# Kernel tuning notes

Measured on AMD Instinct MI355X. Metric: run time of the kernel, lower is better.

The kernel has to match this reference:

```python
import jax, jax.numpy as jnp
from jax import lax
import numpy as np

B, C, H, W = 32, 256, 16, 16          # batch, planes, feature-map HxW
NBUF, REPS, LAB = 100000, 256, 10     # buffer size, reps dim, label dim
D = REPS + LAB                        # retrieval_data feature dim
DH = 64                               # cross_dim_head (heads=1 -> inner=64)
INNER = DH
EPS = 1e-5


def _ln(x, g, b):
    m = x.mean(-1, keepdims=True)
    v = ((x - m) ** 2).mean(-1, keepdims=True)
    return (x - m) * lax.rsqrt(v + EPS) * g + b


def _conv(x, w):
    return lax.conv_general_dilated(x, w, (1, 1), 'SAME',
                                    dimension_numbers=('NCHW', 'OIHW', 'NCHW'))


def _forward(x, conv1_w, conv2_w, bn1_g, bn1_b, bn2_g, bn2_b, retrieval_data,
             ln_attn_g, ln_attn_b, ln_ctx_g, ln_ctx_b, wq, wk, wv, wqe, wo, bo,
             ln_ff_g, ln_ff_b, w1, b1, w2, b2, topk):
    # eval-mode BatchNorm with running mean=0, var=1
    bn = lambda y, g, b: y * g[None, :, None, None] + b[None, :, None, None]
    out = jax.nn.relu(bn(_conv(x, conv1_w), bn1_g, bn1_b))
    out = bn(_conv(out, conv2_w), bn2_g, bn2_b)
    out = jax.nn.relu(out + x)                        # identity shortcut
    t = out.reshape(B, C, H * W).transpose(0, 2, 1)   # [B, n, C] tokens

    # ---- retrieval cross-attention (PreNorm on x and on context) ----
    xn = _ln(t, ln_attn_g, ln_attn_b)
    ctx = _ln(retrieval_data, ln_ctx_g, ln_ctx_b)     # [NBUF, D]
    q = xn @ wq                                        # [B, n, INNER]
    emb = q @ wqe                                      # [B, n, REPS]
    e0 = emb[:, 0, :]                                  # original loop only uses position 0
    buf_reps = ctx[:, :REPS]                           # [NBUF, REPS]
    # squared L2 has the same ordering as the L2 norm used by torch.topk(largest=False)
    dist2 = jnp.sum((buf_reps[None] - e0[:, None]) ** 2, axis=-1)  # [B, NBUF]
    idx = lax.top_k(-dist2, topk)[1]                   # [B, topk] nearest indices
    retrieved = jnp.take(ctx, idx, axis=0)             # [B, topk, D]; identical for all n positions
    reps_r, labels_r = retrieved[..., :REPS], retrieved[..., REPS:]
    k = reps_r @ wk                                    # reps_for_k: K from reps  [B, topk, INNER]
    v = labels_r @ wv                                  # V from labels            [B, topk, INNER]
    sim = jnp.einsum('bnd,bjd->bnj', q, k) * DH ** -0.5
    attn = jax.nn.softmax(sim, axis=-1)
    o = jnp.einsum('bnj,bjd->bnd', attn, v)
    t = o @ wo + bo + t

    # ---- feed-forward (PreNorm, GEGLU, mult=1) ----
    h = _ln(t, ln_ff_g, ln_ff_b) @ w1 + b1             # [B, n, 2C]
    a, g = jnp.split(h, 2, axis=-1)
    t = (a * jax.nn.gelu(g, approximate=False)) @ w2 + b2 + t

    return t.transpose(0, 2, 1).reshape(B, C, H, W)


def setup_inputs() -> dict:
    key = jax.random.key(0)
    ks = jax.random.split(key, 12)
    s = 0.02
    return {
        'x': jax.random.normal(ks[0], (B, C, H, W), jnp.float32),
        'conv1_w': jax.random.normal(ks[1], (C, C, 3, 3), jnp.float32) * s,
        'conv2_w': jax.random.normal(ks[2], (C, C, 3, 3), jnp.float32) * s,
        'bn1_g': jnp.ones((C,), jnp.float32), 'bn1_b': jnp.zeros((C,), jnp.float32),
        'bn2_g': jnp.ones((C,), jnp.float32), 'bn2_b': jnp.zeros((C,), jnp.float32),
        'retrieval_data': jax.random.normal(ks[3], (NBUF, D), jnp.float32),
        'ln_attn_g': jnp.ones((C,), jnp.float32), 'ln_attn_b': jnp.zeros((C,), jnp.float32),
        'ln_ctx_g': jnp.ones((D,), jnp.float32), 'ln_ctx_b': jnp.zeros((D,), jnp.float32),
        'wq': jax.random.normal(ks[4], (C, INNER), jnp.float32) * s,
        'wk': jax.random.normal(ks[5], (REPS, INNER), jnp.float32) * s,
        'wv': jax.random.normal(ks[6], (LAB, INNER), jnp.float32) * s,
        'wqe': jax.random.normal(ks[7], (INNER, REPS), jnp.float32) * s,
        'wo': jax.random.normal(ks[8], (INNER, C), jnp.float32) * s,
        'bo': jnp.zeros((C,), jnp.float32),
        'ln_ff_g': jnp.ones((C,), jnp.float32), 'ln_ff_b': jnp.zeros((C,), jnp.float32),
        'w1': jax.random.normal(ks[9], (C, 2 * C), jnp.float32) * s,
        'b1': jnp.zeros((2 * C,), jnp.float32),
        'w2': jax.random.normal(ks[10], (C, C), jnp.float32) * s,
        'b2': jnp.zeros((C,), jnp.float32),
        'topk': 32,
    }


def reference(x, conv1_w, conv2_w, bn1_g, bn1_b, bn2_g, bn2_b, retrieval_data,
              ln_attn_g, ln_attn_b, ln_ctx_g, ln_ctx_b, wq, wk, wv, wqe, wo, bo,
              ln_ff_g, ln_ff_b, w1, b1, w2, b2, topk):
    return _forward(x, conv1_w, conv2_w, bn1_g, bn1_b, bn2_g, bn2_b, retrieval_data,
                    ln_attn_g, ln_attn_b, ln_ctx_g, ln_ctx_b, wq, wk, wv, wqe, wo, bo,
                    ln_ff_g, ln_ff_b, w1, b1, w2, b2, topk)
```

## Files before the change

kernel.cpp:

```cpp
#include <hip/hip_runtime.h>
#include <hip/hip_bf16.h>
#include <math.h>

#define DEV __device__ __forceinline__

typedef __attribute__((ext_vector_type(8))) short bf16x8;
typedef __attribute__((ext_vector_type(4))) float f32x4;
typedef __attribute__((ext_vector_type(4))) unsigned int u32x4;
typedef __attribute__((ext_vector_type(2))) unsigned int u32x2;

DEV float b2f(unsigned int u) { return __uint_as_float(u << 16); }
DEV unsigned short f2b(float f) {
    unsigned int x = __float_as_uint(f);
    unsigned int r = x + 0x7fffu + ((x >> 16) & 1u);
    return (unsigned short)(r >> 16);
}
DEV unsigned int pack2(float a, float b) {
    return (unsigned int)f2b(a) | ((unsigned int)f2b(b) << 16);
}
DEV float gelu_exact(float g) {
    return 0.5f * g * (1.f + erff(g * 0.70710678118654752f));
}

constexpr size_t WP1  = 0;
// ... 170 lines not shown
        float g = bng[co], bb = bnb[co];
#pragma unroll
        for (int r = 0; r < 4; ++r) {
            int m = m0 + mt * 16 + lq * 4 + r;
            int h = m >> 4, w = m & 15;
            float v = sum[r] * g + bb;
            if (EPI == 0) {
                v = fmaxf(v, 0.f);
                outP[((size_t)img * 324 + (h + 1) * 18 + (w + 1)) * 256 + co] = f2b(v);
            } else {
                v += b2f(resid[((size_t)img * 324 + (h + 1) * 18 + (w + 1)) * 256 + co]);
                v = fmaxf(v, 0.f);
                outT[((size_t)img * 256 + m) * 256 + co] = v;
            }
        }
    }
}

__global__ __launch_bounds__(256) void lnq_k(
    const float* __restrict__ t, const float* __restrict__ g, const float* __restrict__ bta,
    const unsigned short* __restrict__ bpq, const float* __restrict__ wqe,
    unsigned short* __restrict__ qb, unsigned short* __restrict__ e0p)
{
    __shared__ __align__(16) unsigned int frag[64 * 132];
    __shared__ float qrow[64];
    int bx = blockIdx.x, tid = threadIdx.x;
    int wv = tid >> 6, lane = tid & 63;
    int c = lane * 4;
    f32x4 gv = *(const f32x4*)(g + c);
    f32x4 bv = *(const f32x4*)(bta + c);
#pragma unroll
    for (int p = 0; p < 16; ++p) {
        int rl = wv * 16 + p;
        f32x4 x = *(const f32x4*)(t + (size_t)(bx * 64 + rl) * 256 + c);
        float s  = x[0] + x[1] + x[2] + x[3];
        float ss = x[0]*x[0] + x[1]*x[1] + x[2]*x[2] + x[3]*x[3];
#pragma unroll
        for (int off = 32; off >= 1; off >>= 1) { s += __shfl_xor(s, off); ss += __shfl_xor(ss, off); }
        float mean = s * (1.f / 256.f);
        float var  = ss * (1.f / 256.f) - mean * mean;
        float rstd = rsqrtf(fmaxf(var, 0.f) + 1e-5f);
        float y0 = (x[0]-mean)*rstd*gv[0] + bv[0];
        float y1 = (x[1]-mean)*rstd*gv[1] + bv[1];
        float y2 = (x[2]-mean)*rstd*gv[2] + bv[2];
        float y3 = (x[3]-mean)*rstd*gv[3] + bv[3];
        frag[rl * 132 + 2 * lane]     = pack2(y0, y1);
        frag[rl * 132 + 2 * lane + 1] = pack2(y2, y3);
    }
    __syncthreads();
    int lq = lane >> 4, lr = lane & 15;
    f32x4 acc[4];
#pragma unroll
    for (int nt = 0; nt < 4; ++nt) acc[nt] = 0.f;
    const short* sA = (const short*)frag;
#pragma unroll
    for (int kc = 0; kc < 8; ++kc) {
        bf16x8 a = *(const bf16x8*)(sA + (wv * 16 + lr) * 264 + kc * 32 + lq * 8);
#pragma unroll
        for (int nt = 0; nt < 4; ++nt) {
            bf16x8 bfr = *(const bf16x8*)(bpq + (size_t)(kc * 4 + nt) * 512 + lane * 8);
            acc[nt] = __builtin_amdgcn_mfma_f32_16x16x32_bf16(a, bfr, acc[nt], 0, 0, 0);
        }
    }
#pragma unroll
    for (int nt = 0; nt < 4; ++nt)
#pragma unroll
        for (int r = 0; r < 4; ++r)
            qb[(size_t)(bx * 64 + wv * 16 + lq * 4 + r) * 64 + nt * 16 + lr] = f2b(acc[nt][r]);
    if ((bx & 3) == 0 && wv == 0 && lq == 0) {
#pragma unroll
        for (int nt = 0; nt < 4; ++nt) qrow[nt * 16 + lr] = acc[nt][0];
    }
    __syncthreads();
    if ((bx & 3) == 0) {
        int b = bx >> 2;
        int r = tid;
        float a2 = 0.f;
#pragma unroll 8
        for (int d = 0; d < 64; ++d) a2 += qrow[d] * wqe[d * 256 + r];
        int nt = b >> 4, kc = r >> 5;
        int ln_ = (b & 15) + (((r >> 3) & 3) << 4);
        int j = r & 7;
        e0p[(((nt * 8 + kc) * 64) + ln_) * 8 + j] = f2b(a2);
    }
}

__global__ __launch_bounds__(256, 4) void lndist_k(
    const float* __restrict__ ctx, const float* __restrict__ lgam, const float* __restrict__ lbet,
    const unsigned short* __restrict__ e0p, float* __restrict__ dist)
{
    __shared__ __align__(16) unsigned int frag[32 * 132];
    __shared__ __align__(16) float rn2s[32];
    int r0 = blockIdx.x * 32;
    int tid = threadIdx.x;
    int wv = tid >> 6, lane = tid & 63;

    float2 d0[8], d1[8], d2[8];
    const float* base = ctx + (size_t)(r0 + wv * 8) * 266;
#pragma unroll
    for (int p = 0; p < 8; ++p) {
        const float* rowp = base + p * 266;
        d0[p] = *(const float2*)(rowp + 2 * lane);
        d1[p] = *(const float2*)(rowp + 128 + 2 * lane);
        if (lane < 5) d2[p] = *(const float2*)(rowp + 256 + 2 * lane);
        else { d2[p].x = 0.f; d2[p].y = 0.f; }
    }
    float2 g0 = *(const float2*)(lgam + 2 * lane);
    float2 g1 = *(const float2*)(lgam + 128 + 2 * lane);
    float2 b0 = *(const float2*)(lbet + 2 * lane);
    float2 b1 = *(const float2*)(lbet + 128 + 2 * lane);

#pragma unroll
    for (int p = 0; p < 8; ++p) {
        int rl = wv * 8 + p;
        float s  = d0[p].x + d0[p].y + d1[p].x + d1[p].y + d2[p].x + d2[p].y;
        float ss = d0[p].x*d0[p].x + d0[p].y*d0[p].y + d1[p].x*d1[p].x + d1[p].y*d1[p].y
                 + d2[p].x*d2[p].x + d2[p].y*d2[p].y;
#pragma unroll
        for (int off = 32; off >= 1; off >>= 1) { s += __shfl_xor(s, off); ss += __shfl_xor(ss, off); }
        float mean = s * (1.f / 266.f);
        float var  = ss * (1.f / 266.f) - mean * mean;
        float rstd = rsqrtf(fmaxf(var, 0.f) + 1e-5f);
        float c0 = (d0[p].x - mean) * rstd * g0.x + b0.x;
        float c1 = (d0[p].y - mean) * rstd * g0.y + b0.y;
        float c2 = (d1[p].x - mean) * rstd * g1.x + b1.x;
        float c3 = (d1[p].y - mean) * rstd * g1.y + b1.y;
        frag[rl * 132 + lane]      = pack2(c0, c1);
        frag[rl * 132 + 64 + lane] = pack2(c2, c3);
        float nsq = c0*c0 + c1*c1 + c2*c2 + c3*c3;
#pragma unroll
        for (int off = 32; off >= 1; off >>= 1) nsq += __shfl_xor(nsq, off);
        if (lane == 0) rn2s[rl] = nsq;
    }
    __syncthreads();

    int lq = lane >> 4, lr = lane & 15;
    int rt = wv & 1, ch = wv >> 1;
    f32x4 acc = 0.f;
    const short* sA = (const short*)frag;
#pragma unroll
    for (int kc = 0; kc < 8; ++kc) {
        bf16x8 a = *(const bf16x8*)(sA + (rt * 16 + lr) * 264 + kc * 32 + lq * 8);
        bf16x8 b = *(const bf16x8*)(e0p + ((ch * 8 + kc) * 64 + lane) * 8);
        acc = __builtin_amdgcn_mfma_f32_16x16x32_bf16(a, b, acc, 0, 0, 0);
    }
    int mbase = r0 + rt * 16 + lq * 4;
    f32x4 rv = *(f32x4*)(rn2s + rt * 16 + lq * 4);
    f32x4 o;
#pragma unroll
    for (int r = 0; r < 4; ++r) o[r] = rv[r] - 2.f * acc[r];
    *(f32x4*)(dist + (size_t)(ch * 16 + lr) * 100000 + mbase) = o;
}

__global__ __launch_bounds__(256) void topk1(const float* __restrict__ dist,
                                             float* __restrict__ candv,
                                             int* __restrict__ candi)
{
    __shared__ float sv[6250];
    __shared__ float wvv[4]; __shared__ int wvi[4];
    int c = blockIdx.x, b = blockIdx.y;
    int tid = threadIdx.x;
    const float* src = dist + (size_t)b * 100000 + c * 6250;
    for (int i = tid; i < 6250; i += 256) sv[i] = src[i];
    __syncthreads();
    for (int it = 0; it < 32; ++it) {
        float lm = 3e38f; int li = 0;
        for (int i = tid; i < 6250; i += 256) {
            float v = sv[i];
            if (v < lm) { lm = v; li = i; }
        }
#pragma unroll
        for (int off = 32; off >= 1; off >>= 1) {
            float ov = __shfl_xor(lm, off);
            int oi = __shfl_xor(li, off);
            if (ov < lm) { lm = ov; li = oi; }
        }
        if ((tid & 63) == 0) { wvv[tid >> 6] = lm; wvi[tid >> 6] = li; }
        __syncthreads();
        if (tid == 0) {
            float m = wvv[0]; int mi = wvi[0];
#pragma unroll
            for (int w = 1; w < 4; ++w) if (wvv[w] < m) { m = wvv[w]; mi = wvi[w]; }
            candv[((size_t)b * 16 + c) * 32 + it] = m;
            candi[((size_t)b * 16 + c) * 32 + it] = c * 6250 + mi;
            sv[mi] = 3e38f;
        }
        __syncthreads();
    }
}

__global__ __launch_bounds__(256) void topk2(const float* __restrict__ candv,
                                             const int* __restrict__ candi,
                                             int* __restrict__ idxo)
{
    __shared__ float sv[512]; __shared__ int si[512];
    __shared__ float wvv[4]; __shared__ int wvi[4];
    int b = blockIdx.x, tid = threadIdx.x;
    for (int i = tid; i < 512; i += 256) { sv[i] = candv[(size_t)b * 512 + i]; si[i] = candi[(size_t)b * 512 + i]; }
    __syncthreads();
    for (int it = 0; it < 32; ++it) {
        float lm = 3e38f; int li = 0;
#pragma unroll
        for (int rep = 0; rep < 2; ++rep) {
            int i = tid + rep * 256;
            float v = sv[i];
            if (v < lm) { lm = v; li = i; }
        }
#pragma unroll
        for (int off = 32; off >= 1; off >>= 1) {
            float ov = __shfl_xor(lm, off);
            int oi = __shfl_xor(li, off);
            if (ov < lm) { lm = ov; li = oi; }
        }
        if ((tid & 63) == 0) { wvv[tid >> 6] = lm; wvi[tid >> 6] = li; }
        __syncthreads();
        if (tid == 0) {
            float m = wvv[0]; int mi = wvi[0];
#pragma unroll
            for (int w = 1; w < 4; ++w) if (wvv[w] < m) { m = wvv[w]; mi = wvi[w]; }
            idxo[b * 32 + it] = si[mi];
            sv[mi] = 3e38f;
        }
        __syncthreads();
    }
}

__global__ __launch_bounds__(64) void gather_kv(const float* __restrict__ ctx,
                                                const float* __restrict__ g,
                                                const float* __restrict__ b,
                                                const int* __restrict__ idxb,
                                                const float* __restrict__ wk,
                                                const float* __restrict__ wvm,
                                                float* __restrict__ kb,
                                                float* __restrict__ vb)
{
    __shared__ float cnv[266];
    int bj = blockIdx.x;
    int lane = threadIdx.x;
    int row = idxb[bj];
    const float* p = ctx + (size_t)row * 266;
    float2 a0 = *(const float2*)(p + 2 * lane);
    float2 a1 = *(const float2*)(p + 128 + 2 * lane);
    float x4 = 0.f, x5 = 0.f;
    if (lane < 5) { float2 a2 = *(const float2*)(p + 256 + 2 * lane); x4 = a2.x; x5 = a2.y; }
    float s  = a0.x + a0.y + a1.x + a1.y + x4 + x5;
    float ss = a0.x*a0.x + a0.y*a0.y + a1.x*a1.x + a1.y*a1.y + x4*x4 + x5*x5;
#pragma unroll
    for (int off = 32; off >= 1; off >>= 1) { s += __shfl_xor(s, off); ss += __shfl_xor(ss, off); }
    float mean = s * (1.f / 266.f);
    float var  = ss * (1.f / 266.f) - mean * mean;
    float rstd = rsqrtf(fmaxf(var, 0.f) + 1e-5f);
    float2 g0 = *(const float2*)(g + 2 * lane);
    float2 g1 = *(const float2*)(g + 128 + 2 * lane);
    float2 b0 = *(const float2*)(b + 2 * lane);
    float2 b1 = *(const float2*)(b + 128 + 2 * lane);
    cnv[2*lane]       = (a0.x - mean) * rstd * g0.x + b0.x;
    cnv[2*lane + 1]   = (a0.y - mean) * rstd * g0.y + b0.y;
    cnv[128 + 2*lane] = (a1.x - mean) * rstd * g1.x + b1.x;
    cnv[129 + 2*lane] = (a1.y - mean) * rstd * g1.y + b1.y;
    if (lane < 5) {
        float2 g2 = *(const float2*)(g + 256 + 2 * lane);
        float2 b2 = *(const float2*)(b + 256 + 2 * lane);
        cnv[256 + 2*lane] = (x4 - mean) * rstd * g2.x + b2.x;
        cnv[257 + 2*lane] = (x5 - mean) * rstd * g2.y + b2.y;
    }
    __syncthreads();
    float acc = 0.f;
#pragma unroll 8
    for (int r = 0; r < 256; ++r) acc += cnv[r] * wk[r * 64 + lane];
    kb[(size_t)bj * 64 + lane] = acc;
    float acc2 = 0.f;
#pragma unroll
    for (int r = 0; r < 10; ++r) acc2 += cnv[256 + r] * wvm[r * 64 + lane];
    vb[(size_t)bj * 64 + lane] = acc2;
}

__global__ __launch_bounds__(256) void attn_k(const unsigned short* __restrict__ q,
                                              const float* __restrict__ kb,
                                              const float* __restrict__ vb,
                                              unsigned short* __restrict__ ob)
{
    __shared__ float kl[32 * 66];
    __shared__ float vl[32 * 66];
    __shared__ float ql[8 * 64];
    __shared__ float pl[8 * 32];
    int b = blockIdx.x >> 5, pxg = blockIdx.x & 31;
    int px_base = pxg * 8;
    int tid = threadIdx.x;

    for (int i = tid; i < 2048; i += 256) {
        int row = i >> 6, d = i & 63;
        kl[row * 66 + d] = kb[(size_t)b * 2048 + i];
        vl[row * 66 + d] = vb[(size_t)b * 2048 + i];
    }
    for (int i = tid; i < 512; i += 256) {
        ql[i] = b2f(q[((size_t)b * 256 + px_base) * 64 + i]);
    }
    __syncthreads();

    int wv = tid >> 6, lane = tid & 63;
    int lp = wv * 2 + (lane >> 5);
    int j = lane & 31;

    const float* qp = ql + lp * 64;
    const float* kp = kl + j * 66;
    float s = 0.f;
#pragma unroll
    for (int d = 0; d < 64; ++d) s += qp[d] * kp[d];
    s *= 0.125f;

    float mx = s;
#pragma unroll
    for (int off = 16; off >= 1; off >>= 1) mx = fmaxf(mx, __shfl_xor(mx, off));
    float p = expf(s - mx);
    float sum = p;
#pragma unroll
    for (int off = 16; off >= 1; off >>= 1) sum += __shfl_xor(sum, off);
    p /= sum;
    pl[lp * 32 + j] = p;

    int d0 = 2 * j;
    float o0 = 0.f, o1 = 0.f;
#pragma unroll
    for (int jj = 0; jj < 32; ++jj) {
        float pj = pl[lp * 32 + jj];
        float2 vv = *(const float2*)(vl + jj * 66 + d0);
        o0 += pj * vv.x;
        o1 += pj * vv.y;
    }
    ((unsigned int*)ob)[(((size_t)b * 256 + px_base + lp) * 64 + d0) >> 1] = pack2(o0, o1);
}

__global__ __launch_bounds__(256) void wo_ln_k(
    const unsigned short* __restrict__ A, const unsigned short* __restrict__ Bp,
    const float* __restrict__ bo, const float* __restrict__ tres,
    float* __restrict__ t2, unsigned short* __restrict__ xn2,
    const float* __restrict__ lng, const float* __restrict__ lnb)
{
    __shared__ __align__(16) float tile[32 * 268];
    int m0 = blockIdx.x * 32;
    int tid = threadIdx.x, wv = tid >> 6, lane = tid & 63, lq = lane >> 4, lr = lane & 15;
    int n0 = wv * 64;
    f32x4 acc[2][4];
#pragma unroll
    for (int i = 0; i < 2; ++i)
#pragma unroll
        for (int j = 0; j < 4; ++j) acc[i][j] = 0.f;
    const unsigned short* a0p = A + (size_t)(m0 + lr) * 64 + lq * 8;
#pragma unroll
    for (int kc = 0; kc < 2; ++kc) {
        bf16x8 a0 = *(const bf16x8*)(a0p + kc * 32);
        bf16x8 a1 = *(const bf16x8*)(a0p + 16 * 64 + kc * 32);
#pragma unroll
        for (int nt = 0; nt < 4; ++nt) {
            bf16x8 bfr = *(const bf16x8*)(Bp + (size_t)(kc * 16 + (n0 >> 4) + nt) * 512 + lane * 8);
            acc[0][nt] = __builtin_amdgcn_mfma_f32_16x16x32_bf16(a0, bfr, acc[0][nt], 0, 0, 0);
            acc[1][nt] = __builtin_amdgcn_mfma_f32_16x16x32_bf16(a1, bfr, acc[1][nt], 0, 0, 0);
        }
    }
#pragma unroll
    for (int mt = 0; mt < 2; ++mt)
#pragma unroll
        for (int nt = 0; nt < 4; ++nt)
#pragma unroll
            for (int r = 0; r < 4; ++r)
                tile[(mt * 16 + lq * 4 + r) * 268 + n0 + nt * 16 + lr] = acc[mt][nt][r];
    __syncthreads();
    int row = tid >> 3, c0 = (tid & 7) * 32;
    const float* trp = tres + (size_t)(m0 + row) * 256 + c0;
    float v[32];
#pragma unroll
    for (int i = 0; i < 8; ++i) {
        f32x4 t4 = *(f32x4*)(tile + row * 268 + c0 + i * 4);
        f32x4 rr = *(const f32x4*)(trp + i * 4);
        f32x4 bb = *(const f32x4*)(bo + c0 + i * 4);
#pragma unroll
        for (int k = 0; k < 4; ++k) v[i*4+k] = t4[k] + rr[k] + bb[k];
    }
    float* t2p = t2 + (size_t)(m0 + row) * 256 + c0;
#pragma unroll
    for (int i = 0; i < 8; ++i) {
        f32x4 o; o[0] = v[i*4]; o[1] = v[i*4+1]; o[2] = v[i*4+2]; o[3] = v[i*4+3];
        *(f32x4*)(t2p + i * 4) = o;
    }
    float s = 0.f, ss = 0.f;
#pragma unroll
    for (int i = 0; i < 32; ++i) { s += v[i]; ss += v[i] * v[i]; }
#pragma unroll
    for (int off = 1; off <= 4; off <<= 1) { s += __shfl_xor(s, off); ss += __shfl_xor(ss, off); }
    float mean = s * (1.f / 256.f);
    float var  = ss * (1.f / 256.f) - mean * mean;
    float rstd = rsqrtf(fmaxf(var, 0.f) + 1e-5f);
    unsigned int pk[16];
#pragma unroll
    for (int i = 0; i < 16; ++i) {
        float y0 = (v[2*i]   - mean) * rstd * lng[c0+2*i]   + lnb[c0+2*i];
        float y1 = (v[2*i+1] - mean) * rstd * lng[c0+2*i+1] + lnb[c0+2*i+1];
        pk[i] = pack2(y0, y1);
    }
    u32x4* dp = (u32x4*)(xn2 + (size_t)(m0 + row) * 256 + c0);
#pragma unroll
    for (int i = 0; i < 4; ++i) {
        u32x4 o; o.x = pk[i*4]; o.y = pk[i*4+1]; o.z = pk[i*4+2]; o.w = pk[i*4+3];
        dp[i] = o;
    }
}

__global__ __launch_bounds__(256) void ff1_k(
    const unsigned short* __restrict__ A, const unsigned short* __restrict__ Bp,
    const float* __restrict__ b1, unsigned short* __restrict__ u)
{
    __shared__ __align__(16) float tile[64 * 68];
    int m0 = blockIdx.x * 64, by = blockIdx.y;
    int tid = threadIdx.x, wv = tid >> 6, lane = tid & 63, lq = lane >> 4, lr = lane & 15;
    int mh = wv & 1, sel = wv >> 1;
    int m0w = m0 + mh * 32;
    int nbase = sel * 256 + by * 32;
    f32x4 acc[2][2];
#pragma unroll
    for (int i = 0; i < 2; ++i)
#pragma unroll
        for (int j = 0; j < 2; ++j) acc[i][j] = 0.f;
    const unsigned short* a0p = A + (size_t)(m0w + lr) * 256 + lq * 8;
#pragma unroll
    for (int kc = 0; kc < 8; ++kc) {
        bf16x8 a0 = *(const bf16x8*)(a0p + kc * 32);
        bf16x8 a1 = *(const bf16x8*)(a0p + 16 * 256 + kc * 32);
#pragma unroll
        for (int nt = 0; nt < 2; ++nt) {
            bf16x8 bfr = *(const bf16x8*)(Bp + (size_t)(kc * 32 + (nbase >> 4) + nt) * 512 + lane * 8);
            acc[0][nt] = __builtin_amdgcn_mfma_f32_16x16x32_bf16(a0, bfr, acc[0][nt], 0, 0, 0);
            acc[1][nt] = __builtin_amdgcn_mfma_f32_16x16x32_bf16(a1, bfr, acc[1][nt], 0, 0, 0);
        }
    }
#pragma unroll
    for (int nt = 0; nt < 2; ++nt) {
        float bias = b1[nbase + nt * 16 + lr];
#pragma unroll
        for (int mt = 0; mt < 2; ++mt)
#pragma unroll
            for (int r = 0; r < 4; ++r)
                tile[(mh * 32 + mt * 16 + lq * 4 + r) * 68 + sel * 32 + nt * 16 + lr] = acc[mt][nt][r] + bias;
    }
    __syncthreads();
    int row = tid >> 2, c0 = (tid & 3) * 8;
    unsigned int pk[4];
#pragma unroll
    for (int i = 0; i < 4; ++i) {
        float a0 = tile[row * 68 + c0 + 2*i];
        float a1 = tile[row * 68 + c0 + 2*i + 1];
        float g0 = tile[row * 68 + 32 + c0 + 2*i];
        float g1 = tile[row * 68 + 32 + c0 + 2*i + 1];
        pk[i] = pack2(a0 * gelu_exact(g0), a1 * gelu_exact(g1));
    }
    u32x4 o; o.x = pk[0]; o.y = pk[1]; o.z = pk[2]; o.w = pk[3];
    *(u32x4*)(u + (size_t)(m0 + row) * 256 + by * 32 + c0) = o;
}

__global__ __launch_bounds__(256) void ff2_k(
    const unsigned short* __restrict__ A, const unsigned short* __restrict__ Bp,
    const float* __restrict__ b2, const float* __restrict__ t2,
    float* __restrict__ out)
{
    __shared__ __align__(16) float tile[64 * 68];
    int m0 = blockIdx.x * 64, n0 = blockIdx.y * 64;
    int tid = threadIdx.x, wv = tid >> 6, lane = tid & 63, lq = lane >> 4, lr = lane & 15;
    int mq = wv & 1, nq = wv >> 1;
    int m0w = m0 + mq * 32, n0w = n0 + nq * 32;
    f32x4 acc[2][2];
#pragma unroll
    for (int i = 0; i < 2; ++i)
#pragma unroll
        for (int j = 0; j < 2; ++j) acc[i][j] = 0.f;
    const unsigned short* a0p = A + (size_t)(m0w + lr) * 256 + lq * 8;
#pragma unroll
    for (int kc = 0; kc < 8; ++kc) {
        bf16x8 a0 = *(const bf16x8*)(a0p + kc * 32);
        bf16x8 a1 = *(const bf16x8*)(a0p + 16 * 256 + kc * 32);
#pragma unroll
        for (int nt = 0; nt < 2; ++nt) {
            bf16x8 bfr = *(const bf16x8*)(Bp + (size_t)(kc * 16 + (n0w >> 4) + nt) * 512 + lane * 8);
            acc[0][nt] = __builtin_amdgcn_mfma_f32_16x16x32_bf16(a0, bfr, acc[0][nt], 0, 0, 0);
            acc[1][nt] = __builtin_amdgcn_mfma_f32_16x16x32_bf16(a1, bfr, acc[1][nt], 0, 0, 0);
        }
    }
#pragma unroll
    for (int nt = 0; nt < 2; ++nt) {
        int col = n0w + nt * 16 + lr;
        float bv = b2[col];
#pragma unroll
        for (int mt = 0; mt < 2; ++mt)
#pragma unroll
            for (int r = 0; r < 4; ++r) {
                int m = m0w + mt * 16 + lq * 4 + r;
                tile[(mq * 32 + mt * 16 + lq * 4 + r) * 68 + nq * 32 + nt * 16 + lr] =
                    acc[mt][nt][r] + bv + t2[(size_t)m * 256 + col];
            }
    }
    __syncthreads();
    int b = m0 >> 8, px0 = m0 & 255;
    int cl = tid >> 2, pc = (tid & 3) * 16;
    float* dp = out + ((size_t)b * 256 + n0 + cl) * 256 + px0 + pc;
#pragma unroll
    for (int i = 0; i < 4; ++i) {
        f32x4 o;
        o[0] = tile[(pc + i * 4 + 0) * 68 + cl];
        o[1] = tile[(pc + i * 4 + 1) * 68 + cl];
        o[2] = tile[(pc + i * 4 + 2) * 68 + cl];
        o[3] = tile[(pc + i * 4 + 3) * 68 + cl];
        *(f32x4*)(dp + i * 4) = o;
    }
}

extern "C" void kernel_launch(void* const* d_in, const int* in_sizes, int n_in,
                              void* d_out, int out_size, void* d_ws, size_t ws_size,
                              hipStream_t stream)
{
    (void)in_sizes; (void)n_in; (void)out_size; (void)ws_size;
    const float* x    = (const float*)d_in[0];
    const float* c1w  = (const float*)d_in[1];
    const float* c2w  = (const float*)d_in[2];
    const float* bn1g = (const float*)d_in[3];
    const float* bn1b = (const float*)d_in[4];
    const float* bn2g = (const float*)d_in[5];
    const float* bn2b = (const float*)d_in[6];
    const float* rdat = (const float*)d_in[7];
    const float* lag  = (const float*)d_in[8];
    const float* labp = (const float*)d_in[9];
    const float* lcg  = (const float*)d_in[10];
    const float* lcb  = (const float*)d_in[11];
    const float* wq   = (const float*)d_in[12];
    const float* wk   = (const float*)d_in[13];
    const float* wv   = (const float*)d_in[14];
    const float* wqe  = (const float*)d_in[15];
    const float* wo   = (const float*)d_in[16];
    const float* bo   = (const float*)d_in[17];
    const float* lfg  = (const float*)d_in[18];
    const float* lfb  = (const float*)d_in[19];
    const float* w1   = (const float*)d_in[20];
    const float* b1   = (const float*)d_in[21];
    const float* w2   = (const float*)d_in[22];
    const float* b2   = (const float*)d_in[23];

    char* ws = (char*)d_ws;
    unsigned short* wp1  = (unsigned short*)(ws + WP1);
    unsigned short* wp2  = (unsigned short*)(ws + WP2);
    unsigned short* bpq  = (unsigned short*)(ws + BPQ);
    unsigned short* bpo  = (unsigned short*)(ws + BPO);
    unsigned short* bp1  = (unsigned short*)(ws + BP1);
    unsigned short* bp2  = (unsigned short*)(ws + BP2);
    unsigned short* xtp  = (unsigned short*)(ws + XTP);
    unsigned short* o1p  = (unsigned short*)(ws + O1P);
    float*          tb   = (float*)(ws + TBUF);
    unsigned short* qb   = (unsigned short*)(ws + QB);
    unsigned short* e0p  = (unsigned short*)(ws + E0P);
    float*          dist = (float*)(ws + DIST);
    float*          cdv  = (float*)(ws + CANDV);
    int*            cdi  = (int*)(ws + CANDI);
    int*            idxb = (int*)(ws + IDXB);
    float*          kb   = (float*)(ws + KBF);
    float*          vbuf = (float*)(ws + VBF);
    unsigned short* ob   = (unsigned short*)(ws + OBF);
    float*          t2   = (float*)(ws + T2B);
    unsigned short* xn2  = (unsigned short*)(ws + XN2);
    unsigned short* ub   = (unsigned short*)(ws + UBF);
    float*          outp = (float*)d_out;

    setup_k<<<944, 256, 0, stream>>>(x, c1w, c2w, wq, wo, w1, w2,
                                     wp1, wp2, bpq, bpo, bp1, bp2, xtp, o1p);
    conv_mfma<0><<<512, 256, 0, stream>>>(xtp, wp1, bn1g, bn1b, nullptr, o1p, nullptr);
    conv_mfma<1><<<512, 256, 0, stream>>>(o1p, wp2, bn2g, bn2b, xtp, nullptr, tb);
    lnq_k<<<128, 256, 0, stream>>>(tb, lag, labp, bpq, wqe, qb, e0p);
    lndist_k<<<3125, 256, 0, stream>>>(rdat, lcg, lcb, e0p, dist);
    topk1<<<dim3(16, 32), 256, 0, stream>>>(dist, cdv, cdi);
    topk2<<<32, 256, 0, stream>>>(cdv, cdi, idxb);
    gather_kv<<<1024, 64, 0, stream>>>(rdat, lcg, lcb, idxb, wk, wv, kb, vbuf);
    attn_k<<<1024, 256, 0, stream>>>(qb, kb, vbuf, ob);
    wo_ln_k<<<256, 256, 0, stream>>>(ob, bpo, bo, tb, t2, xn2, lfg, lfb);
    ff1_k<<<dim3(128, 8), 256, 0, stream>>>(xn2, bp1, b1, ub);
    ff2_k<<<dim3(128, 4), 256, 0, stream>>>(ub, bp2, b2, t2, outp);
}
```

Measured before the change: 397.7 us.

## Use per-wave top-k selection and fuse select/gather and the FFN tail

The first top-k stage now lets each of the four waves in a block pick its own 32 smallest values from a 1600-element slice, using only wave barriers. This removes the per-iteration block barriers and the serial thread-0 merge, at the cost of four times as many candidates. The second top-k stage, the context LayerNorm gather and the K/V projections are merged into one kernel per batch, and the K projection reuses each weight load across 8 rows. The Wo projection with residual and LayerNorm, FF1 with GELU gating, and FF2 with residual and transposed store are fused into one kernel that keeps intermediates in LDS. This cuts launches and global round trips, but the fused tail runs only 256 blocks and uses more LDS per block.

```diff
diff --git a/kernel.cpp b/kernel.cpp
--- a/kernel.cpp
+++ b/kernel.cpp
@@ -346,20 +346,26 @@
     *(f32x4*)(dist + (size_t)(ch * 16 + lr) * 100000 + mbase) = o;
 }
 
-__global__ __launch_bounds__(256) void topk1(const float* __restrict__ dist,
-                                             float* __restrict__ candv,
-                                             int* __restrict__ candi)
-{
-    __shared__ float sv[6250];
-    __shared__ float wvv[4]; __shared__ int wvi[4];
+__global__ __launch_bounds__(256) void topk1w(const float* __restrict__ dist,
+                                              float* __restrict__ candv,
+                                              int* __restrict__ candi)
+{
+    __shared__ float sv[6400];
     int c = blockIdx.x, b = blockIdx.y;
     int tid = threadIdx.x;
+    int wv = tid >> 6, lane = tid & 63;
     const float* src = dist + (size_t)b * 100000 + c * 6250;
     for (int i = tid; i < 6250; i += 256) sv[i] = src[i];
-    __syncthreads();
+    for (int i = 6250 + tid; i < 6400; i += 256) sv[i] = 3e38f;
+    __syncthreads();
+    int base = wv * 1600;
+    float* cvp = candv + (((size_t)b * 16 + c) * 4 + wv) * 32;
+    int*   cip = candi + (((size_t)b * 16 + c) * 4 + wv) * 32;
     for (int it = 0; it < 32; ++it) {
-        float lm = 3e38f; int li = 0;
-        for (int i = tid; i < 6250; i += 256) {
+        float lm = 3e38f; int li = base;
+#pragma unroll
+        for (int t = 0; t < 25; ++t) {
+            int i = base + lane + t * 64;
             float v = sv[i];
             if (v < lm) { lm = v; li = i; }
         }
@@ -369,104 +375,135 @@
             int oi = __shfl_xor(li, off);
             if (ov < lm) { lm = ov; li = oi; }
         }
-        if ((tid & 63) == 0) { wvv[tid >> 6] = lm; wvi[tid >> 6] = li; }
-        __syncthreads();
-        if (tid == 0) {
-            float m = wvv[0]; int mi = wvi[0];
-#pragma unroll
-            for (int w = 1; w < 4; ++w) if (wvv[w] < m) { m = wvv[w]; mi = wvi[w]; }
-            candv[((size_t)b * 16 + c) * 32 + it] = m;
-            candi[((size_t)b * 16 + c) * 32 + it] = c * 6250 + mi;
-            sv[mi] = 3e38f;
-        }
-        __syncthreads();
-    }
-}
-
-__global__ __launch_bounds__(256) void topk2(const float* __restrict__ candv,
-                                             const int* __restrict__ candi,
-                                             int* __restrict__ idxo)
-{
-    __shared__ float sv[512]; __shared__ int si[512];
-    __shared__ float wvv[4]; __shared__ int wvi[4];
+        if (lane == 0) {
+            cvp[it] = lm;
+            cip[it] = c * 6250 + li;
+            sv[li] = 3e38f;
+        }
+        __builtin_amdgcn_wave_barrier();
+    }
+}
+
+__global__ __launch_bounds__(256) void selkv_k(const float* __restrict__ candv,
+                                               const int* __restrict__ candi,
+                                               const float* __restrict__ ctx,
+                                               const float* __restrict__ g,
+                                               const float* __restrict__ bta,
+                                               const float* __restrict__ wk,
+                                               const float* __restrict__ wvm,
+                                               float* __restrict__ kb,
+                                               float* __restrict__ vb)
+{
+    __shared__ float sv[2048]; __shared__ int si[2048];
+    __shared__ float fv[128];  __shared__ int fi[128];
+    __shared__ int rows[32];
+    __shared__ float cnv[32][268];
     int b = blockIdx.x, tid = threadIdx.x;
-    for (int i = tid; i < 512; i += 256) { sv[i] = candv[(size_t)b * 512 + i]; si[i] = candi[(size_t)b * 512 + i]; }
-    __syncthreads();
-    for (int it = 0; it < 32; ++it) {
-        float lm = 3e38f; int li = 0;
-#pragma unroll
-        for (int rep = 0; rep < 2; ++rep) {
-            int i = tid + rep * 256;
-            float v = sv[i];
-            if (v < lm) { lm = v; li = i; }
-        }
-#pragma unroll
-        for (int off = 32; off >= 1; off >>= 1) {
-            float ov = __shfl_xor(lm, off);
-            int oi = __shfl_xor(li, off);
-            if (ov < lm) { lm = ov; li = oi; }
-        }
-        if ((tid & 63) == 0) { wvv[tid >> 6] = lm; wvi[tid >> 6] = li; }
-        __syncthreads();
-        if (tid == 0) {
-            float m = wvv[0]; int mi = wvi[0];
-#pragma unroll
-            for (int w = 1; w < 4; ++w) if (wvv[w] < m) { m = wvv[w]; mi = wvi[w]; }
-            idxo[b * 32 + it] = si[mi];
-            sv[mi] = 3e38f;
-        }
-        __syncthreads();
-    }
-}
-
-__global__ __launch_bounds__(64) void gather_kv(const float* __restrict__ ctx,
-                                                const float* __restrict__ g,
-                                                const float* __restrict__ b,
-                                                const int* __restrict__ idxb,
-                                                const float* __restrict__ wk,
-                                                const float* __restrict__ wvm,
-                                                float* __restrict__ kb,
-                                                float* __restrict__ vb)
-{
-    __shared__ float cnv[266];
-    int bj = blockIdx.x;
-    int lane = threadIdx.x;
-    int row = idxb[bj];
-    const float* p = ctx + (size_t)row * 266;
-    float2 a0 = *(const float2*)(p + 2 * lane);
-    float2 a1 = *(const float2*)(p + 128 + 2 * lane);
-    float x4 = 0.f, x5 = 0.f;
-    if (lane < 5) { float2 a2 = *(const float2*)(p + 256 + 2 * lane); x4 = a2.x; x5 = a2.y; }
-    float s  = a0.x + a0.y + a1.x + a1.y + x4 + x5;
-    float ss = a0.x*a0.x + a0.y*a0.y + a1.x*a1.x + a1.y*a1.y + x4*x4 + x5*x5;
-#pragma unroll
-    for (int off = 32; off >= 1; off >>= 1) { s += __shfl_xor(s, off); ss += __shfl_xor(ss, off); }
-    float mean = s * (1.f / 266.f);
-    float var  = ss * (1.f / 266.f) - mean * mean;
-    float rstd = rsqrtf(fmaxf(var, 0.f) + 1e-5f);
-    float2 g0 = *(const float2*)(g + 2 * lane);
-    float2 g1 = *(const float2*)(g + 128 + 2 * lane);
-    float2 b0 = *(const float2*)(b + 2 * lane);
-    float2 b1 = *(const float2*)(b + 128 + 2 * lane);
-    cnv[2*lane]       = (a0.x - mean) * rstd * g0.x + b0.x;
-    cnv[2*lane + 1]   = (a0.y - mean) * rstd * g0.y + b0.y;
-    cnv[128 + 2*lane] = (a1.x - mean) * rstd * g1.x + b1.x;
-    cnv[129 + 2*lane] = (a1.y - mean) * rstd * g1.y + b1.y;
-    if (lane < 5) {
-        float2 g2 = *(const float2*)(g + 256 + 2 * lane);
-        float2 b2 = *(const float2*)(b + 256 + 2 * lane);
-        cnv[256 + 2*lane] = (x4 - mean) * rstd * g2.x + b2.x;
-        cnv[257 + 2*lane] = (x5 - mean) * rstd * g2.y + b2.y;
-    }
-    __syncthreads();
-    float acc = 0.f;
-#pragma unroll 8
-    for (int r = 0; r < 256; ++r) acc += cnv[r] * wk[r * 64 + lane];
-    kb[(size_t)bj * 64 + lane] = acc;
-    float acc2 = 0.f;
-#pragma unroll
-    for (int r = 0; r < 10; ++r) acc2 += cnv[256 + r] * wvm[r * 64 + lane];
-    vb[(size_t)bj * 64 + lane] = acc2;
+    int wv = tid >> 6, lane = tid & 63;
+    for (int i = tid; i < 2048; i += 256) {
+        sv[i] = candv[(size_t)b * 2048 + i];
+        si[i] = candi[(size_t)b * 2048 + i];
+    }
+    __syncthreads();
+    {
+        int base = wv * 512;
+        for (int it = 0; it < 32; ++it) {
+            float lm = 3e38f; int li = base;
+#pragma unroll
+            for (int t = 0; t < 8; ++t) {
+                int i = base + lane + t * 64;
+                float v = sv[i];
+                if (v < lm) { lm = v; li = i; }
+            }
+#pragma unroll
+            for (int off = 32; off >= 1; off >>= 1) {
+                float ov = __shfl_xor(lm, off);
+                int oi = __shfl_xor(li, off);
+                if (ov < lm) { lm = ov; li = oi; }
+            }
+            if (lane == 0) { fv[wv * 32 + it] = lm; fi[wv * 32 + it] = si[li]; sv[li] = 3e38f; }
+            __builtin_amdgcn_wave_barrier();
+        }
+    }
+    __syncthreads();
+    if (wv == 0) {
+        for (int it = 0; it < 32; ++it) {
+            float lm = 3e38f; int li = 0;
+#pragma unroll
+            for (int t = 0; t < 2; ++t) {
+                int i = lane + t * 64;
+                float v = fv[i];
+                if (v < lm) { lm = v; li = i; }
+            }
+#pragma unroll
+            for (int off = 32; off >= 1; off >>= 1) {
+                float ov = __shfl_xor(lm, off);
+                int oi = __shfl_xor(li, off);
+                if (ov < lm) { lm = ov; li = oi; }
+            }
+            if (lane == 0) { rows[it] = fi[li]; fv[li] = 3e38f; }
+            __builtin_amdgcn_wave_barrier();
+        }
+    }
+    __syncthreads();
+    for (int p = 0; p < 8; ++p) {
+        int j = wv * 8 + p;
+        int rrow = rows[j];
+        const float* pp = ctx + (size_t)rrow * 266;
+        float2 a0 = *(const float2*)(pp + 2 * lane);
+        float2 a1 = *(const float2*)(pp + 128 + 2 * lane);
+        float x4 = 0.f, x5 = 0.f;
+        if (lane < 5) { float2 a2 = *(const float2*)(pp + 256 + 2 * lane); x4 = a2.x; x5 = a2.y; }
+        float s  = a0.x + a0.y + a1.x + a1.y + x4 + x5;
+        float ss = a0.x*a0.x + a0.y*a0.y + a1.x*a1.x + a1.y*a1.y + x4*x4 + x5*x5;
+#pragma unroll
+        for (int off = 32; off >= 1; off >>= 1) { s += __shfl_xor(s, off); ss += __shfl_xor(ss, off); }
+        float mean = s * (1.f / 266.f);
+        float var  = ss * (1.f / 266.f) - mean * mean;
+        float rstd = rsqrtf(fmaxf(var, 0.f) + 1e-5f);
+        float2 g0 = *(const float2*)(g + 2 * lane);
+        float2 g1 = *(const float2*)(g + 128 + 2 * lane);
+        float2 b0 = *(const float2*)(bta + 2 * lane);
+        float2 b1 = *(const float2*)(bta + 128 + 2 * lane);
+        cnv[j][2*lane]       = (a0.x - mean) * rstd * g0.x + b0.x;
+        cnv[j][2*lane + 1]   = (a0.y - mean) * rstd * g0.y + b0.y;
+        cnv[j][128 + 2*lane] = (a1.x - mean) * rstd * g1.x + b1.x;
+        cnv[j][129 + 2*lane] = (a1.y - mean) * rstd * g1.y + b1.y;
+        if (lane < 5) {
+            float2 g2 = *(const float2*)(g + 256 + 2 * lane);
+            float2 b2 = *(const float2*)(bta + 256 + 2 * lane);
+            cnv[j][256 + 2*lane] = (x4 - mean) * rstd * g2.x + b2.x;
+            cnv[j][257 + 2*lane] = (x5 - mean) * rstd * g2.y + b2.y;
+        }
+    }
+    __syncthreads();
+    {
+        float acc[8];
+#pragma unroll
+        for (int p = 0; p < 8; ++p) acc[p] = 0.f;
+        int j0 = wv * 8;
+        for (int r = 0; r < 256; r += 4) {
+            float w0 = wk[(r + 0) * 64 + lane];
+            float w1_ = wk[(r + 1) * 64 + lane];
+            float w2_ = wk[(r + 2) * 64 + lane];
+            float w3 = wk[(r + 3) * 64 + lane];
+#pragma unroll
+            for (int p = 0; p < 8; ++p) {
+                f32x4 cv = *(const f32x4*)&cnv[j0 + p][r];
+                acc[p] += cv[0] * w0 + cv[1] * w1_ + cv[2] * w2_ + cv[3] * w3;
+            }
+        }
+#pragma unroll
+        for (int p = 0; p < 8; ++p)
+            kb[((size_t)b * 32 + j0 + p) * 64 + lane] = acc[p];
+#pragma unroll
+        for (int p = 0; p < 8; ++p) {
+            float a2 = 0.f;
+#pragma unroll
+            for (int r = 0; r < 10; ++r) a2 += cnv[j0 + p][256 + r] * wvm[r * 64 + lane];
+            vb[((size_t)b * 32 + j0 + p) * 64 + lane] = a2;
+        }
+    }
 }
 
 __global__ __launch_bounds__(256) void attn_k(const unsigned short* __restrict__ q,
@@ -525,184 +562,171 @@
     ((unsigned int*)ob)[(((size_t)b * 256 + px_base + lp) * 64 + d0) >> 1] = pack2(o0, o1);
 }
 
-__global__ __launch_bounds__(256) void wo_ln_k(
-    const unsigned short* __restrict__ A, const unsigned short* __restrict__ Bp,
+__global__ __launch_bounds__(256) void tail_k(
+    const unsigned short* __restrict__ A,
+    const unsigned short* __restrict__ Bpo,
     const float* __restrict__ bo, const float* __restrict__ tres,
-    float* __restrict__ t2, unsigned short* __restrict__ xn2,
-    const float* __restrict__ lng, const float* __restrict__ lnb)
+    const float* __restrict__ lng, const float* __restrict__ lnb,
+    const unsigned short* __restrict__ Bp1, const float* __restrict__ b1,
+    const unsigned short* __restrict__ Bp2, const float* __restrict__ b2,
+    float* __restrict__ out)
 {
     __shared__ __align__(16) float tile[32 * 268];
+    __shared__ __align__(16) unsigned short xt[32 * 264];
     int m0 = blockIdx.x * 32;
     int tid = threadIdx.x, wv = tid >> 6, lane = tid & 63, lq = lane >> 4, lr = lane & 15;
     int n0 = wv * 64;
-    f32x4 acc[2][4];
+    const short* xts = (const short*)xt;
+
+    {
+        f32x4 acc[2][4];
+#pragma unroll
+        for (int i = 0; i < 2; ++i)
+#pragma unroll
+            for (int j = 0; j < 4; ++j) acc[i][j] = 0.f;
+        const unsigned short* a0p = A + (size_t)(m0 + lr) * 64 + lq * 8;
+#pragma unroll
+        for (int kc = 0; kc < 2; ++kc) {
+            bf16x8 a0 = *(const bf16x8*)(a0p + kc * 32);
+            bf16x8 a1 = *(const bf16x8*)(a0p + 16 * 64 + kc * 32);
+#pragma unroll
+            for (int nt = 0; nt < 4; ++nt) {
+                bf16x8 bfr = *(const bf16x8*)(Bpo + (size_t)(kc * 16 + (n0 >> 4) + nt) * 512 + lane * 8);
+                acc[0][nt] = __builtin_amdgcn_mfma_f32_16x16x32_bf16(a0, bfr, acc[0][nt], 0, 0, 0);
+                acc[1][nt] = __builtin_amdgcn_mfma_f32_16x16x32_bf16(a1, bfr, acc[1][nt], 0, 0, 0);
+            }
+        }
+#pragma unroll
+        for (int mt = 0; mt < 2; ++mt)
+#pragma unroll
+            for (int nt = 0; nt < 4; ++nt)
+#pragma unroll
+                for (int r = 0; r < 4; ++r)
+                    tile[(mt * 16 + lq * 4 + r) * 268 + n0 + nt * 16 + lr] = acc[mt][nt][r];
+    }
+    __syncthreads();
+
+    {
+        int row = tid >> 3, c0 = (tid & 7) * 32;
+        const float* trp = tres + (size_t)(m0 + row) * 256 + c0;
+        float v[32];
+#pragma unroll
+        for (int i = 0; i < 8; ++i) {
+            f32x4 t4 = *(f32x4*)(tile + row * 268 + c0 + i * 4);
+            f32x4 rr = *(const f32x4*)(trp + i * 4);
+            f32x4 bb = *(const f32x4*)(bo + c0 + i * 4);
+#pragma unroll
+            for (int k = 0; k < 4; ++k) v[i*4+k] = t4[k] + rr[k] + bb[k];
+        }
+#pragma unroll
+        for (int i = 0; i < 8; ++i) {
+            f32x4 o; o[0] = v[i*4]; o[1] = v[i*4+1]; o[2] = v[i*4+2]; o[3] = v[i*4+3];
+            *(f32x4*)(tile + row * 268 + c0 + i * 4) = o;
+        }
+        float s = 0.f, ss = 0.f;
+#pragma unroll
+        for (int i = 0; i < 32; ++i) { s += v[i]; ss += v[i] * v[i]; }
+#pragma unroll
+        for (int off = 1; off <= 4; off <<= 1) { s += __shfl_xor(s, off); ss += __shfl_xor(ss, off); }
+        float mean = s * (1.f / 256.f);
+        float var  = ss * (1.f / 256.f) - mean * mean;
+        float rstd = rsqrtf(fmaxf(var, 0.f) + 1e-5f);
+        unsigned int pk[16];
+#pragma unroll
+        for (int i = 0; i < 16; ++i) {
+            float y0 = (v[2*i]   - mean) * rstd * lng[c0+2*i]   + lnb[c0+2*i];
+            float y1 = (v[2*i+1] - mean) * rstd * lng[c0+2*i+1] + lnb[c0+2*i+1];
+            pk[i] = pack2(y0, y1);
+        }
+        u32x4* dp = (u32x4*)(xt + row * 264 + c0);
+#pragma unroll
+        for (int i = 0; i < 4; ++i) {
+            u32x4 o; o.x = pk[i*4]; o.y = pk[i*4+1]; o.z = pk[i*4+2]; o.w = pk[i*4+3];
+            dp[i] = o;
+        }
+    }
+    __syncthreads();
+
+    f32x4 fa[2][4], fg[2][4];
 #pragma unroll
     for (int i = 0; i < 2; ++i)
 #pragma unroll
-        for (int j = 0; j < 4; ++j) acc[i][j] = 0.f;
-    const unsigned short* a0p = A + (size_t)(m0 + lr) * 64 + lq * 8;
-#pragma unroll
-    for (int kc = 0; kc < 2; ++kc) {
-        bf16x8 a0 = *(const bf16x8*)(a0p + kc * 32);
-        bf16x8 a1 = *(const bf16x8*)(a0p + 16 * 64 + kc * 32);
+        for (int j = 0; j < 4; ++j) { fa[i][j] = 0.f; fg[i][j] = 0.f; }
+#pragma unroll
+    for (int kc = 0; kc < 8; ++kc) {
+        bf16x8 a0 = *(const bf16x8*)(xts + lr * 264 + kc * 32 + lq * 8);
+        bf16x8 a1 = *(const bf16x8*)(xts + (16 + lr) * 264 + kc * 32 + lq * 8);
 #pragma unroll
         for (int nt = 0; nt < 4; ++nt) {
-            bf16x8 bfr = *(const bf16x8*)(Bp + (size_t)(kc * 16 + (n0 >> 4) + nt) * 512 + lane * 8);
-            acc[0][nt] = __builtin_amdgcn_mfma_f32_16x16x32_bf16(a0, bfr, acc[0][nt], 0, 0, 0);
-            acc[1][nt] = __builtin_amdgcn_mfma_f32_16x16x32_bf16(a1, bfr, acc[1][nt], 0, 0, 0);
-        }
-    }
-#pragma unroll
-    for (int mt = 0; mt < 2; ++mt)
-#pragma unroll
-        for (int nt = 0; nt < 4; ++nt)
-#pragma unroll
-            for (int r = 0; r < 4; ++r)
-                tile[(mt * 16 + lq * 4 + r) * 268 + n0 + nt * 16 + lr] = acc[mt][nt][r];
-    __syncthreads();
-    int row = tid >> 3, c0 = (tid & 7) * 32;
-    const float* trp = tres + (size_t)(m0 + row) * 256 + c0;
-    float v[32];
-#pragma unroll
-    for (int i = 0; i < 8; ++i) {
-        f32x4 t4 = *(f32x4*)(tile + row * 268 + c0 + i * 4);
-        f32x4 rr = *(const f32x4*)(trp + i * 4);
-        f32x4 bb = *(const f32x4*)(bo + c0 + i * 4);
-#pragma unroll
-        for (int k = 0; k < 4; ++k) v[i*4+k] = t4[k] + rr[k] + bb[k];
-    }
-    float* t2p = t2 + (size_t)(m0 + row) * 256 + c0;
-#pragma unroll
-    for (int i = 0; i < 8; ++i) {
-        f32x4 o; o[0] = v[i*4]; o[1] = v[i*4+1]; o[2] = v[i*4+2]; o[3] = v[i*4+3];
-        *(f32x4*)(t2p + i * 4) = o;
-    }
-    float s = 0.f, ss = 0.f;
-#pragma unroll
-    for (int i = 0; i < 32; ++i) { s += v[i]; ss += v[i] * v[i]; }
-#pragma unroll
-    for (int off = 1; off <= 4; off <<= 1) { s += __shfl_xor(s, off); ss += __shfl_xor(ss, off); }
-    float mean = s * (1.f / 256.f);
-    float var  = ss * (1.f / 256.f) - mean * mean;
-    float rstd = rsqrtf(fmaxf(var, 0.f) + 1e-5f);
-    unsigned int pk[16];
-#pragma unroll
-    for (int i = 0; i < 16; ++i) {
-        float y0 = (v[2*i]   - mean) * rstd * lng[c0+2*i]   + lnb[c0+2*i];
-        float y1 = (v[2*i+1] - mean) * rstd * lng[c0+2*i+1] + lnb[c0+2*i+1];
-        pk[i] = pack2(y0, y1);
-    }
-    u32x4* dp = (u32x4*)(xn2 + (size_t)(m0 + row) * 256 + c0);
-#pragma unroll
-    for (int i = 0; i < 4; ++i) {
-        u32x4 o; o.x = pk[i*4]; o.y = pk[i*4+1]; o.z = pk[i*4+2]; o.w = pk[i*4+3];
-        dp[i] = o;
-    }
-}
-
-__global__ __launch_bounds__(256) void ff1_k(
-    const unsigned short* __restrict__ A, const unsigned short* __restrict__ Bp,
-    const float* __restrict__ b1, unsigned short* __restrict__ u)
-{
-    __shared__ __align__(16) float tile[64 * 68];
-    int m0 = blockIdx.x * 64, by = blockIdx.y;
-    int tid = threadIdx.x, wv = tid >> 6, lane = tid & 63, lq = lane >> 4, lr = lane & 15;
-    int mh = wv & 1, sel = wv >> 1;
-    int m0w = m0 + mh * 32;
-    int nbase = sel * 256 + by * 32;
-    f32x4 acc[2][2];
-#pragma unroll
-    for (int i = 0; i < 2; ++i)
-#pragma unroll
-        for (int j = 0; j < 2; ++j) acc[i][j] = 0.f;
-    const unsigned short* a0p = A + (size_t)(m0w + lr) * 256 + lq * 8;
-#pragma unroll
-    for (int kc = 0; kc < 8; ++kc) {
-        bf16x8 a0 = *(const bf16x8*)(a0p + kc * 32);
-        bf16x8 a1 = *(const bf16x8*)(a0p + 16 * 256 + kc * 32);
-#pragma unroll
-        for (int nt = 0; nt < 2; ++nt) {
-            bf16x8 bfr = *(const bf16x8*)(Bp + (size_t)(kc * 32 + (nbase >> 4) + nt) * 512 + lane * 8);
-            acc[0][nt] = __builtin_amdgcn_mfma_f32_16x16x32_bf16(a0, bfr, acc[0][nt], 0, 0, 0);
-            acc[1][nt] = __builtin_amdgcn_mfma_f32_16x16x32_bf16(a1, bfr, acc[1][nt], 0, 0, 0);
-        }
-    }
-#pragma unroll
-    for (int nt = 0; nt < 2; ++nt) {
-        float bias = b1[nbase + nt * 16 + lr];
+            bf16x8 bA = *(const bf16x8*)(Bp1 + (size_t)(kc * 32 + (n0 >> 4) + nt) * 512 + lane * 8);
+            bf16x8 bG = *(const bf16x8*)(Bp1 + (size_t)(kc * 32 + 16 + (n0 >> 4) + nt) * 512 + lane * 8);
+            fa[0][nt] = __builtin_amdgcn_mfma_f32_16x16x32_bf16(a0, bA, fa[0][nt], 0, 0, 0);
+            fa[1][nt] = __builtin_amdgcn_mfma_f32_16x16x32_bf16(a1, bA, fa[1][nt], 0, 0, 0);
+            fg[0][nt] = __builtin_amdgcn_mfma_f32_16x16x32_bf16(a0, bG, fg[0][nt], 0, 0, 0);
+            fg[1][nt] = __builtin_amdgcn_mfma_f32_16x16x32_bf16(a1, bG, fg[1][nt], 0, 0, 0);
+        }
+    }
+    __syncthreads();
+#pragma unroll
+    for (int nt = 0; nt < 4; ++nt) {
+        int col = n0 + nt * 16 + lr;
+        float ba = b1[col], bg = b1[256 + col];
 #pragma unroll
         for (int mt = 0; mt < 2; ++mt)
 #pragma unroll
-            for (int r = 0; r < 4; ++r)
-                tile[(mh * 32 + mt * 16 + lq * 4 + r) * 68 + sel * 32 + nt * 16 + lr] = acc[mt][nt][r] + bias;
-    }
-    __syncthreads();
-    int row = tid >> 2, c0 = (tid & 3) * 8;
-    unsigned int pk[4];
-#pragma unroll
-    for (int i = 0; i < 4; ++i) {
-        float a0 = tile[row * 68 + c0 + 2*i];
-        float a1 = tile[row * 68 + c0 + 2*i + 1];
-        float g0 = tile[row * 68 + 32 + c0 + 2*i];
-        float g1 = tile[row * 68 + 32 + c0 + 2*i + 1];
-        pk[i] = pack2(a0 * gelu_exact(g0), a1 * gelu_exact(g1));
-    }
-    u32x4 o; o.x = pk[0]; o.y = pk[1]; o.z = pk[2]; o.w = pk[3];
-    *(u32x4*)(u + (size_t)(m0 + row) * 256 + by * 32 + c0) = o;
-}
-
-__global__ __launch_bounds__(256) void ff2_k(
-    const unsigned short* __restrict__ A, const unsigned short* __restrict__ Bp,
-    const float* __restrict__ b2, const float* __restrict__ t2,
-    float* __restrict__ out)
-{
-    __shared__ __align__(16) float tile[64 * 68];
-    int m0 = blockIdx.x * 64, n0 = blockIdx.y * 64;
-    int tid = threadIdx.x, wv = tid >> 6, lane = tid & 63, lq = lane >> 4, lr = lane & 15;
-    int mq = wv & 1, nq = wv >> 1;
-    int m0w = m0 + mq * 32, n0w = n0 + nq * 32;
-    f32x4 acc[2][2];
-#pragma unroll
-    for (int i = 0; i < 2; ++i)
-#pragma unroll
-        for (int j = 0; j < 2; ++j) acc[i][j] = 0.f;
-    const unsigned short* a0p = A + (size_t)(m0w + lr) * 256 + lq * 8;
-#pragma unroll
-    for (int kc = 0; kc < 8; ++kc) {
-        bf16x8 a0 = *(const bf16x8*)(a0p + kc * 32);
-        bf16x8 a1 = *(const bf16x8*)(a0p + 16 * 256 + kc * 32);
-#pragma unroll
-        for (int nt = 0; nt < 2; ++nt) {
-            bf16x8 bfr = *(const bf16x8*)(Bp + (size_t)(kc * 16 + (n0w >> 4) + nt) * 512 + lane * 8);
-            acc[0][nt] = __builtin_amdgcn_mfma_f32_16x16x32_bf16(a0, bfr, acc[0][nt], 0, 0, 0);
-            acc[1][nt] = __builtin_amdgcn_mfma_f32_16x16x32_bf16(a1, bfr, acc[1][nt], 0, 0, 0);
-        }
-    }
-#pragma unroll
-    for (int nt = 0; nt < 2; ++nt) {
-        int col = n0w + nt * 16 + lr;
-        float bv = b2[col];
-#pragma unroll
-        for (int mt = 0; mt < 2; ++mt)
-#pragma unroll
             for (int r = 0; r < 4; ++r) {
-                int m = m0w + mt * 16 + lq * 4 + r;
-                tile[(mq * 32 + mt * 16 + lq * 4 + r) * 68 + nq * 32 + nt * 16 + lr] =
-                    acc[mt][nt][r] + bv + t2[(size_t)m * 256 + col];
-            }
-    }
-    __syncthreads();
-    int b = m0 >> 8, px0 = m0 & 255;
-    int cl = tid >> 2, pc = (tid & 3) * 16;
-    float* dp = out + ((size_t)b * 256 + n0 + cl) * 256 + px0 + pc;
-#pragma unroll
-    for (int i = 0; i < 4; ++i) {
-        f32x4 o;
-        o[0] = tile[(pc + i * 4 + 0) * 68 + cl];
-        o[1] = tile[(pc + i * 4 + 1) * 68 + cl];
-        o[2] = tile[(pc + i * 4 + 2) * 68 + cl];
-        o[3] = tile[(pc + i * 4 + 3) * 68 + cl];
-        *(f32x4*)(dp + i * 4) = o;
+                float a = fa[mt][nt][r] + ba;
+                float gg = fg[mt][nt][r] + bg;
+                xt[(mt * 16 + lq * 4 + r) * 264 + col] = f2b(a * gelu_exact(gg));
+            }
+    }
+    __syncthreads();
+
+    {
+        f32x4 c2[2][4];
+#pragma unroll
+        for (int i = 0; i < 2; ++i)
+#pragma unroll
+            for (int j = 0; j < 4; ++j) c2[i][j] = 0.f;
+#pragma unroll
+        for (int kc = 0; kc < 8; ++kc) {
+            bf16x8 a0 = *(const bf16x8*)(xts + lr * 264 + kc * 32 + lq * 8);
+            bf16x8 a1 = *(const bf16x8*)(xts + (16 + lr) * 264 + kc * 32 + lq * 8);
+#pragma unroll
+            for (int nt = 0; nt < 4; ++nt) {
+                bf16x8 bfr = *(const bf16x8*)(Bp2 + (size_t)(kc * 16 + (n0 >> 4) + nt) * 512 + lane * 8);
+                c2[0][nt] = __builtin_amdgcn_mfma_f32_16x16x32_bf16(a0, bfr, c2[0][nt], 0, 0, 0);
+                c2[1][nt] = __builtin_amdgcn_mfma_f32_16x16x32_bf16(a1, bfr, c2[1][nt], 0, 0, 0);
+            }
+        }
+#pragma unroll
+        for (int nt = 0; nt < 4; ++nt) {
+            int col = n0 + nt * 16 + lr;
+            float bv = b2[col];
+#pragma unroll
+            for (int mt = 0; mt < 2; ++mt)
+#pragma unroll
+                for (int r = 0; r < 4; ++r) {
+                    int m = mt * 16 + lq * 4 + r;
+                    tile[m * 268 + col] = c2[mt][nt][r] + bv + tile[m * 268 + col];
+                }
+        }
+    }
+    __syncthreads();
+
+    {
+        int b = m0 >> 8, px0 = m0 & 255;
+        int c = tid;
+        float* dp = out + ((size_t)b * 256 + c) * 256 + px0;
+#pragma unroll
+        for (int q = 0; q < 8; ++q) {
+            f32x4 o;
+            o[0] = tile[(q * 4 + 0) * 268 + c];
+            o[1] = tile[(q * 4 + 1) * 268 + c];
+            o[2] = tile[(q * 4 + 2) * 268 + c];
+            o[3] = tile[(q * 4 + 3) * 268 + c];
+            *(f32x4*)(dp + q * 4) = o;
+        }
     }
 }
 
@@ -751,13 +775,9 @@
     float*          dist = (float*)(ws + DIST);
     float*          cdv  = (float*)(ws + CANDV);
     int*            cdi  = (int*)(ws + CANDI);
-    int*            idxb = (int*)(ws + IDXB);
     float*          kb   = (float*)(ws + KBF);
     float*          vbuf = (float*)(ws + VBF);
     unsigned short* ob   = (unsigned short*)(ws + OBF);
-    float*          t2   = (float*)(ws + T2B);
-    unsigned short* xn2  = (unsigned short*)(ws + XN2);
-    unsigned short* ub   = (unsigned short*)(ws + UBF);
     float*          outp = (float*)d_out;
 
     setup_k<<<944, 256, 0, stream>>>(x, c1w, c2w, wq, wo, w1, w2,
@@ -766,11 +786,8 @@
     conv_mfma<1><<<512, 256, 0, stream>>>(o1p, wp2, bn2g, bn2b, xtp, nullptr, tb);
     lnq_k<<<128, 256, 0, stream>>>(tb, lag, labp, bpq, wqe, qb, e0p);
     lndist_k<<<3125, 256, 0, stream>>>(rdat, lcg, lcb, e0p, dist);
-    topk1<<<dim3(16, 32), 256, 0, stream>>>(dist, cdv, cdi);
-    topk2<<<32, 256, 0, stream>>>(cdv, cdi, idxb);
-    gather_kv<<<1024, 64, 0, stream>>>(rdat, lcg, lcb, idxb, wk, wv, kb, vbuf);
+    topk1w<<<dim3(16, 32), 256, 0, stream>>>(dist, cdv, cdi);
+    selkv_k<<<32, 256, 0, stream>>>(cdv, cdi, rdat, lcg, lcb, wk, wv, kb, vbuf);
     attn_k<<<1024, 256, 0, stream>>>(qb, kb, vbuf, ob);
-    wo_ln_k<<<256, 256, 0, stream>>>(ob, bpo, bo, tb, t2, xn2, lfg, lfb);
-    ff1_k<<<dim3(128, 8), 256, 0, stream>>>(xn2, bp1, b1, ub);
-    ff2_k<<<dim3(128, 4), 256, 0, stream>>>(ub, bp2, b2, t2, outp);
-}
+    tail_k<<<256, 256, 0, stream>>>(ob, bpo, bo, tb, lfg, lfb, bp1, b1, bp2, b2, outp);
+}
```

After: 395.3 us. About the same (-0.6%).
